# Kernel tuning notes

Measured on AMD Instinct MI355X. Metric: run time of the kernel, lower is better.

Reference implementation:

```python
import jax, jax.numpy as jnp
import numpy as np

LUT_N = 16 * 17 * 17 * 17  # 78608, covers max index 16*(16*17*17 + 16*17 + 16) = 78592
H = W = 2048


def setup_inputs() -> dict:
    key = jax.random.key(0)
    k1, k2, k3, k4 = jax.random.split(key, 4)
    # quantized pixel values in [0, 16], stored as float like the torch module expects
    x_in = jax.random.randint(k1, (1, 3, H, W), 0, 17).astype(jnp.float32)
    x_s = jax.random.randint(k2, (1, 3, H, W), 0, 17).astype(jnp.float32)
    # int8 LUT tables of shape [N, 20, 1, 1]
    feature_msb = jax.random.randint(k3, (LUT_N, 20, 1, 1), -32, 32).astype(jnp.int8)
    feature_lsb = jax.random.randint(k4, (LUT_N, 20, 1, 1), -32, 32).astype(jnp.int8)
    return {"x_in": x_in, "x_s": x_s, "feature_msb": feature_msb, "feature_lsb": feature_lsb}


def reference(x_in, x_s, feature_msb, feature_lsb):
    B, C, Hh, Ww = x_in.shape
    # index weights: [16*17*17, 16*17, 16], broadcast over (1,3,1,1)
    weights = jnp.array([16 * 17 * 17, 16 * 17, 16], dtype=jnp.float32).reshape(1, 3, 1, 1)
    idx_msb = jnp.sum(x_in * weights, axis=1).reshape(-1).astype(jnp.int32)  # [B*H*W]
    idx_lsb = jnp.sum(x_s * weights, axis=1).reshape(-1).astype(jnp.int32)
    nfeat = feature_msb.shape[1]  # 20
    # gather -> (1, H, W, 20) -> (1, 20, H, W), cast to float as in torch .float()
    out_msb = feature_msb[idx_msb].reshape(1, Hh, Ww, nfeat).transpose(0, 3, 1, 2).astype(jnp.float32)
    out_lsb = feature_lsb[idx_lsb].reshape(1, Hh, Ww, nfeat).transpose(0, 3, 1, 2).astype(jnp.float32)
    out = out_msb + out_lsb
    # AdaptiveAvgPool2d(1) == global mean over H, W
    out = jnp.mean(out, axis=(2, 3), keepdims=True)  # (1, 20, 1, 1)
    # quantize to 0.25 steps and clamp to [-32, 31.75]
    out = jnp.clip(jnp.round(out * 4.0) / 4.0, -32.0, 31.75)
    return out
```

## Files before the change

### kernel.cpp

```cpp
#include <hip/hip_runtime.h>


#define NBINS 4913
#define HPAD  4928
#define NPIX  (2048 * 2048)
#define G4    (NPIX / 4)
#define NFEAT 20
#define BINGRP 154
#define ROWGRP 16

#define PART_OFF 196608
#define HIST_OFF 458752

__global__ __launch_bounds__(256) void compact_k(const int* __restrict__ msb,
                                                 const int* __restrict__ lsb,
                                                 int* __restrict__ cm,
                                                 int* __restrict__ cl) {
    int ok = 1;
    for (int i = 0; i < 64; ++i) {
        int v = msb[i];
        ok &= (v >= -32 && v < 32);
    }
    const bool is_int32 = (ok != 0);

    const int total = NBINS * 5;
    int t = blockIdx.x * 256 + threadIdx.x;
    const int stride = gridDim.x * 256;
    for (; t < total; t += stride) {
        int j = t / 5;
        int k = t - j * 5;
        int wm, wl;
        if (is_int32) {
            const int* rm = msb + j * 320 + k * 4;
            const int* rl = lsb + j * 320 + k * 4;
            unsigned um = (unsigned)(rm[0] & 0xff) | ((unsigned)(rm[1] & 0xff) << 8) |
                          ((unsigned)(rm[2] & 0xff) << 16) | ((unsigned)(rm[3] & 0xff) << 24);
            unsigned ul = (unsigned)(rl[0] & 0xff) | ((unsigned)(rl[1] & 0xff) << 8) |
                          ((unsigned)(rl[2] & 0xff) << 16) | ((unsigned)(rl[3] & 0xff) << 24);
            wm = (int)um;
            wl = (int)ul;
        } else {
            wm = msb[j * 80 + k];
            wl = lsb[j * 80 + k];
        }
        cm[t] = wm;
        cl[t] = wl;
    }
}

__global__ __launch_bounds__(256) void feat_hist(const float* __restrict__ xin,
                                                 const float* __restrict__ xs,
                                                 unsigned* __restrict__ hists) {
    __shared__ int hist[NBINS];
    for (int i = threadIdx.x; i < NBINS; i += 256) hist[i] = 0;
    __syncthreads();

    const float4* a = (const float4*)xin;
    const float4* b = (const float4*)xs;
    const int nt = gridDim.x * 256;
    for (int g = blockIdx.x * 256 + threadIdx.x; g < G4; g += nt) {
        float4 a0 = a[g], a1 = a[g + G4], a2 = a[g + 2 * G4];
        float4 b0 = b[g], b1 = b[g + G4], b2 = b[g + 2 * G4];

        int m0 = (int)fmaf(a0.x, 289.0f, fmaf(a1.x, 17.0f, a2.x));
        int m1 = (int)fmaf(a0.y, 289.0f, fmaf(a1.y, 17.0f, a2.y));
        int m2 = (int)fmaf(a0.z, 289.0f, fmaf(a1.z, 17.0f, a2.z));
        int m3 = (int)fmaf(a0.w, 289.0f, fmaf(a1.w, 17.0f, a2.w));
        int s0 = (int)fmaf(b0.x, 289.0f, fmaf(b1.x, 17.0f, b2.x));
        int s1 = (int)fmaf(b0.y, 289.0f, fmaf(b1.y, 17.0f, b2.y));
        int s2 = (int)fmaf(b0.z, 289.0f, fmaf(b1.z, 17.0f, b2.z));
        int s3 = (int)fmaf(b0.w, 289.0f, fmaf(b1.w, 17.0f, b2.w));

        atomicAdd(&hist[m0], 1);
        atomicAdd(&hist[m1], 1);
        atomicAdd(&hist[m2], 1);
        atomicAdd(&hist[m3], 1);
        atomicAdd(&hist[s0], 1 << 16);
        atomicAdd(&hist[s1], 1 << 16);
        atomicAdd(&hist[s2], 1 << 16);
        atomicAdd(&hist[s3], 1 << 16);
    }
    __syncthreads();

    unsigned* row = hists + (size_t)blockIdx.x * HPAD;
    for (int i = threadIdx.x; i < HPAD; i += 256)
        row[i] = (i < NBINS) ? (unsigned)hist[i] : 0u;
}

__global__ __launch_bounds__(256) void merge_dot_k(const unsigned* __restrict__ hists,
                                                   const int* __restrict__ cm,
                                                   const int* __restrict__ cl,
                                                   int* __restrict__ partial, int nh) {
    __shared__ unsigned part[8][32];
    const int t = threadIdx.x;
    const int s = t >> 5;
    const int bo = t & 31;
    const int j = blockIdx.x * 32 + bo;

    const int rpg = nh / ROWGRP;
    const int r0 = blockIdx.y * rpg;
    const int r1 = r0 + rpg;

    unsigned sum = 0;
    for (int b = r0 + s; b < r1; b += 8)
        sum += hists[(size_t)b * HPAD + j];
    part[s][bo] = sum;
    __syncthreads();

    if (t < 32) {
        unsigned h = 0;
#pragma unroll
        for (int ss = 0; ss < 8; ++ss) h += part[ss][bo];
        int hm = (int)(h & 0xffffu);
        int hl = (int)(h >> 16);

        int acc[NFEAT];
#pragma unroll
        for (int f = 0; f < NFEAT; ++f) acc[f] = 0;
        if (j < NBINS && h != 0u) {
            const int* rm = cm + j * 5;
            const int* rl = cl + j * 5;
#pragma unroll
            for (int k = 0; k < 5; ++k) {
                int wm = rm[k], wl = rl[k];
                acc[4 * k + 0] += hm * ((wm << 24) >> 24) + hl * ((wl << 24) >> 24);
                acc[4 * k + 1] += hm * ((wm << 16) >> 24) + hl * ((wl << 16) >> 24);
                acc[4 * k + 2] += hm * ((wm << 8) >> 24) + hl * ((wl << 8) >> 24);
                acc[4 * k + 3] += hm * (wm >> 24) + hl * (wl >> 24);
            }
        }
#pragma unroll
        for (int f = 0; f < NFEAT; ++f) {
            int v = acc[f];
#pragma unroll
            for (int o = 16; o > 0; o >>= 1) v += __shfl_xor(v, o, 64);
            acc[f] = v;
        }
        if (t == 0) {
            const int row = blockIdx.y * BINGRP + blockIdx.x;
#pragma unroll
            for (int f = 0; f < NFEAT; ++f)
                partial[row * NFEAT + f] = acc[f];
        }
    }
}

__global__ __launch_bounds__(256) void feat_dot(const float* __restrict__ xin,
                                                const float* __restrict__ xs,
                                                const int* __restrict__ cm,
                                                const int* __restrict__ cl,
                                                int* __restrict__ partial) {
    __shared__ int hist[NBINS];
    __shared__ int wsum[4][NFEAT];
    for (int i = threadIdx.x; i < NBINS; i += 256) hist[i] = 0;
    __syncthreads();

    const float4* a = (const float4*)xin;
    const float4* b = (const float4*)xs;
    const int nt = gridDim.x * 256;
    for (int g = blockIdx.x * 256 + threadIdx.x; g < G4; g += nt) {
        float4 a0 = a[g], a1 = a[g + G4], a2 = a[g + 2 * G4];
        float4 b0 = b[g], b1 = b[g + G4], b2 = b[g + 2 * G4];
        int m0 = (int)fmaf(a0.x, 289.0f, fmaf(a1.x, 17.0f, a2.x));
        int m1 = (int)fmaf(a0.y, 289.0f, fmaf(a1.y, 17.0f, a2.y));
        int m2 = (int)fmaf(a0.z, 289.0f, fmaf(a1.z, 17.0f, a2.z));
        int m3 = (int)fmaf(a0.w, 289.0f, fmaf(a1.w, 17.0f, a2.w));
        int s0 = (int)fmaf(b0.x, 289.0f, fmaf(b1.x, 17.0f, b2.x));
        int s1 = (int)fmaf(b0.y, 289.0f, fmaf(b1.y, 17.0f, b2.y));
        int s2 = (int)fmaf(b0.z, 289.0f, fmaf(b1.z, 17.0f, b2.z));
        int s3 = (int)fmaf(b0.w, 289.0f, fmaf(b1.w, 17.0f, b2.w));
        atomicAdd(&hist[m0], 1);
        atomicAdd(&hist[m1], 1);
        atomicAdd(&hist[m2], 1);
        atomicAdd(&hist[m3], 1);
        atomicAdd(&hist[s0], 1 << 16);
        atomicAdd(&hist[s1], 1 << 16);
        atomicAdd(&hist[s2], 1 << 16);
        atomicAdd(&hist[s3], 1 << 16);
    }
    __syncthreads();

    int acc[NFEAT];
#pragma unroll
    for (int f = 0; f < NFEAT; ++f) acc[f] = 0;
    for (int j = threadIdx.x; j < NBINS; j += 256) {
        int h = hist[j];
        int hm = h & 0xffff;
        int hl = (int)((unsigned)h >> 16);
        if (hm) {
            const int* r = cm + j * 5;
#pragma unroll
            for (int k = 0; k < 5; ++k) {
                int w = r[k];
                acc[4 * k + 0] += hm * ((w << 24) >> 24);
                acc[4 * k + 1] += hm * ((w << 16) >> 24);
                acc[4 * k + 2] += hm * ((w << 8) >> 24);
                acc[4 * k + 3] += hm * (w >> 24);
            }
        }
        if (hl) {
            const int* r = cl + j * 5;
#pragma unroll
            for (int k = 0; k < 5; ++k) {
                int w = r[k];
                acc[4 * k + 0] += hl * ((w << 24) >> 24);
                acc[4 * k + 1] += hl * ((w << 16) >> 24);
                acc[4 * k + 2] += hl * ((w << 8) >> 24);
                acc[4 * k + 3] += hl * (w >> 24);
            }
        }
    }

    const int lane = threadIdx.x & 63;
    const int wv = threadIdx.x >> 6;
#pragma unroll
    for (int f = 0; f < NFEAT; ++f) {
        int v = acc[f];
#pragma unroll
        for (int o = 32; o > 0; o >>= 1) v += __shfl_xor(v, o, 64);
        if (lane == 0) wsum[wv][f] = v;
    }
    __syncthreads();
    if (threadIdx.x < NFEAT) {
        int f = threadIdx.x;
        partial[blockIdx.x * NFEAT + f] = wsum[0][f] + wsum[1][f] + wsum[2][f] + wsum[3][f];
    }
}

__global__ __launch_bounds__(64) void finalize_k(const int* __restrict__ partial,
                                                 float* __restrict__ out, int nb) {
    const int f = blockIdx.x;
    const int lane = threadIdx.x;
    int s = 0;
    for (int b = lane; b < nb; b += 64) s += partial[b * NFEAT + f];
#pragma unroll
    for (int o = 32; o > 0; o >>= 1) s += __shfl_xor(s, o, 64);
    if (lane == 0) {
        double m4 = (double)s * (1.0 / 1048576.0);
        double r = rint(m4);
        float v = (float)(r * 0.25);
        v = fminf(fmaxf(v, -32.0f), 31.75f);
        out[f] = v;
    }
}

extern "C" void kernel_launch(void* const* d_in, const int* in_sizes, int n_in,
                              void* d_out, int out_size, void* d_ws, size_t ws_size,
                              hipStream_t stream) {
    const float* xin = (const float*)d_in[0];
    const float* xs = (const float*)d_in[1];
    const int* msb = (const int*)d_in[2];
    const int* lsb = (const int*)d_in[3];
    float* out = (float*)d_out;

    int* cm = (int*)d_ws;
    int* cl = (int*)((char*)d_ws + 98304);
    int* partial = (int*)((char*)d_ws + PART_OFF);
    unsigned* hists = (unsigned*)((char*)d_ws + HIST_OFF);

    const size_t rowb = (size_t)HPAD * 4;
    int nh = 0;
    if (ws_size >= (size_t)HIST_OFF + 2048 * rowb) nh = 2048;
    else if (ws_size >= (size_t)HIST_OFF + 1536 * rowb) nh = 1536;
    else if (ws_size >= (size_t)HIST_OFF + 1024 * rowb) nh = 1024;

    compact_k<<<96, 256, 0, stream>>>(msb, lsb, cm, cl);
    if (nh) {
        feat_hist<<<nh, 256, 0, stream>>>(xin, xs, hists);
        merge_dot_k<<<dim3(BINGRP, ROWGRP), 256, 0, stream>>>(hists, cm, cl, partial, nh);
        finalize_k<<<NFEAT, 64, 0, stream>>>(partial, out, BINGRP * ROWGRP);
    } else {
        feat_dot<<<1024, 256, 0, stream>>>(xin, xs, cm, cl, partial);
        finalize_k<<<NFEAT, 64, 0, stream>>>(partial, out, 1024);
    }
}
```

Measured before the change: 160.9 us.

## Fuse LUT compaction into histogram kernel and fix histogram grid at 1024x512

Folds the compact_k launch into the first 48 blocks of feat_hist, removing one kernel launch and its serialization. Histogram blocks grow to 512 threads and the per-block histogram count is fixed at 1024 instead of being picked from up to 2048 by workspace size. This halves the merge traffic in merge_dot_k but changes shared-memory atomic contention per block. The first blocks now do extra compaction work before histogramming.

```diff
diff --git a/kernel.cpp b/kernel.cpp
--- a/kernel.cpp
+++ b/kernel.cpp
@@ -6,16 +6,19 @@
 #define NPIX  (2048 * 2048)
 #define G4    (NPIX / 4)
 #define NFEAT 20
+#define NH    1024
+#define HT    512
 #define BINGRP 154
 #define ROWGRP 16
 
 #define PART_OFF 196608
 #define HIST_OFF 458752
 
-__global__ __launch_bounds__(256) void compact_k(const int* __restrict__ msb,
-                                                 const int* __restrict__ lsb,
-                                                 int* __restrict__ cm,
-                                                 int* __restrict__ cl) {
+__device__ __forceinline__ void compact_range(const int* __restrict__ msb,
+                                              const int* __restrict__ lsb,
+                                              int* __restrict__ cm,
+                                              int* __restrict__ cl,
+                                              int t0, int stride) {
     int ok = 1;
     for (int i = 0; i < 64; ++i) {
         int v = msb[i];
@@ -24,9 +27,7 @@
     const bool is_int32 = (ok != 0);
 
     const int total = NBINS * 5;
-    int t = blockIdx.x * 256 + threadIdx.x;
-    const int stride = gridDim.x * 256;
-    for (; t < total; t += stride) {
+    for (int t = t0; t < total; t += stride) {
         int j = t / 5;
         int k = t - j * 5;
         int wm, wl;
@@ -48,17 +49,24 @@
     }
 }
 
-__global__ __launch_bounds__(256) void feat_hist(const float* __restrict__ xin,
-                                                 const float* __restrict__ xs,
-                                                 unsigned* __restrict__ hists) {
+__global__ __launch_bounds__(HT) void feat_hist(const float* __restrict__ xin,
+                                                const float* __restrict__ xs,
+                                                const int* __restrict__ msb,
+                                                const int* __restrict__ lsb,
+                                                int* __restrict__ cm,
+                                                int* __restrict__ cl,
+                                                unsigned* __restrict__ hists) {
     __shared__ int hist[NBINS];
-    for (int i = threadIdx.x; i < NBINS; i += 256) hist[i] = 0;
+    for (int i = threadIdx.x; i < NBINS; i += HT) hist[i] = 0;
+
+    if (blockIdx.x < 48)
+        compact_range(msb, lsb, cm, cl, blockIdx.x * HT + threadIdx.x, 48 * HT);
     __syncthreads();
 
     const float4* a = (const float4*)xin;
     const float4* b = (const float4*)xs;
-    const int nt = gridDim.x * 256;
-    for (int g = blockIdx.x * 256 + threadIdx.x; g < G4; g += nt) {
+    const int nt = gridDim.x * HT;
+    for (int g = blockIdx.x * HT + threadIdx.x; g < G4; g += nt) {
         float4 a0 = a[g], a1 = a[g + G4], a2 = a[g + 2 * G4];
         float4 b0 = b[g], b1 = b[g + G4], b2 = b[g + 2 * G4];
 
@@ -83,21 +91,21 @@
     __syncthreads();
 
     unsigned* row = hists + (size_t)blockIdx.x * HPAD;
-    for (int i = threadIdx.x; i < HPAD; i += 256)
+    for (int i = threadIdx.x; i < HPAD; i += HT)
         row[i] = (i < NBINS) ? (unsigned)hist[i] : 0u;
 }
 
 __global__ __launch_bounds__(256) void merge_dot_k(const unsigned* __restrict__ hists,
                                                    const int* __restrict__ cm,
                                                    const int* __restrict__ cl,
-                                                   int* __restrict__ partial, int nh) {
+                                                   int* __restrict__ partial) {
     __shared__ unsigned part[8][32];
     const int t = threadIdx.x;
     const int s = t >> 5;
     const int bo = t & 31;
     const int j = blockIdx.x * 32 + bo;
 
-    const int rpg = nh / ROWGRP;
+    const int rpg = NH / ROWGRP;
     const int r0 = blockIdx.y * rpg;
     const int r1 = r0 + rpg;
 
@@ -143,6 +151,13 @@
                 partial[row * NFEAT + f] = acc[f];
         }
     }
+}
+
+__global__ __launch_bounds__(256) void compact_k(const int* __restrict__ msb,
+                                                 const int* __restrict__ lsb,
+                                                 int* __restrict__ cm,
+                                                 int* __restrict__ cl) {
+    compact_range(msb, lsb, cm, cl, blockIdx.x * 256 + threadIdx.x, gridDim.x * 256);
 }
 
 __global__ __launch_bounds__(256) void feat_dot(const float* __restrict__ xin,
@@ -258,18 +273,13 @@
     int* partial = (int*)((char*)d_ws + PART_OFF);
     unsigned* hists = (unsigned*)((char*)d_ws + HIST_OFF);
 
-    const size_t rowb = (size_t)HPAD * 4;
-    int nh = 0;
-    if (ws_size >= (size_t)HIST_OFF + 2048 * rowb) nh = 2048;
-    else if (ws_size >= (size_t)HIST_OFF + 1536 * rowb) nh = 1536;
-    else if (ws_size >= (size_t)HIST_OFF + 1024 * rowb) nh = 1024;
-
-    compact_k<<<96, 256, 0, stream>>>(msb, lsb, cm, cl);
-    if (nh) {
-        feat_hist<<<nh, 256, 0, stream>>>(xin, xs, hists);
-        merge_dot_k<<<dim3(BINGRP, ROWGRP), 256, 0, stream>>>(hists, cm, cl, partial, nh);
+    const size_t need = (size_t)HIST_OFF + (size_t)NH * HPAD * 4;
+    if (ws_size >= need) {
+        feat_hist<<<NH, HT, 0, stream>>>(xin, xs, msb, lsb, cm, cl, hists);
+        merge_dot_k<<<dim3(BINGRP, ROWGRP), 256, 0, stream>>>(hists, cm, cl, partial);
         finalize_k<<<NFEAT, 64, 0, stream>>>(partial, out, BINGRP * ROWGRP);
     } else {
+        compact_k<<<96, 256, 0, stream>>>(msb, lsb, cm, cl);
         feat_dot<<<1024, 256, 0, stream>>>(xin, xs, cm, cl, partial);
         finalize_k<<<NFEAT, 64, 0, stream>>>(partial, out, 1024);
     }
```

Measured after the change: 149.8 us. -6.9%, faster.
